# Kernel optimization log

Hardware: AMD Instinct MI355X
Metric: run time of the kernel (lower is better)

The kernel has to match this reference:

```python
import jax, jax.numpy as jnp
import numpy as np

N_STEPS, BATCH, N_IN, N_NEURONS, N_OUT = 512, 256, 64, 256, 1


def setup_inputs() -> dict:
    key = jax.random.key(0)
    ks = jax.random.split(key, 12)
    s_in = 1.0 / np.sqrt(N_NEURONS)
    inp = {
        "X": jax.random.normal(ks[0], (N_STEPS, BATCH, N_IN), jnp.float32),
        # nn.RNN (tanh, 1 layer) params
        "W_ih": jax.random.uniform(ks[1], (N_NEURONS, N_IN), jnp.float32, -s_in, s_in),
        "W_hh": jax.random.uniform(ks[2], (N_NEURONS, N_NEURONS), jnp.float32, -s_in, s_in),
        "b_ih": jax.random.uniform(ks[3], (N_NEURONS,), jnp.float32, -s_in, s_in),
        "b_hh": jax.random.uniform(ks[4], (N_NEURONS,), jnp.float32, -s_in, s_in),
        # nn.RNNCell params
        "Wc_ih": jax.random.uniform(ks[5], (N_NEURONS, N_NEURONS), jnp.float32, -s_in, s_in),
        "Wc_hh": jax.random.uniform(ks[6], (N_NEURONS, N_NEURONS), jnp.float32, -s_in, s_in),
        "bc_ih": jax.random.uniform(ks[7], (N_NEURONS,), jnp.float32, -s_in, s_in),
        "bc_hh": jax.random.uniform(ks[8], (N_NEURONS,), jnp.float32, -s_in, s_in),
        # fc params
        "W_fc": jax.random.uniform(ks[9], (N_OUT, N_NEURONS), jnp.float32, -s_in, s_in),
        "b_fc": jax.random.uniform(ks[10], (N_OUT,), jnp.float32, -s_in, s_in),
    }
    return inp


def reference(X, W_ih, W_hh, b_ih, b_hh, Wc_ih, Wc_hh, bc_ih, bc_hh, W_fc, b_fc):
    batch = X.shape[1]
    n_neurons = W_hh.shape[0]

    # --- rnn_pre: single-layer tanh RNN over time (h0 = zeros) ---
    def rnn_step(h, x_t):
        h_new = jnp.tanh(x_t @ W_ih.T + b_ih + h @ W_hh.T + b_hh)
        return h_new, h_new

    h0 = jnp.zeros((batch, n_neurons), X.dtype)
    _, out_pre = jax.lax.scan(rnn_step, h0, X)  # (S, B, N)

    # --- attention loop, n_neurons iterations, sequential dependency ---
    def att_step(hp, _):
        # pre_soft = sum(out_pre * hidden_post, 2) -> (S, B)
        pre_soft = jnp.einsum("sbn,bn->sb", out_pre, hp)
        # softmax over dim 0 (time)
        post_soft = jax.nn.softmax(pre_soft, axis=0)
        # attention = sum over time of out_pre weighted by post_soft -> (B, N)
        attention = jnp.einsum("sbn,sb->bn", out_pre, post_soft)
        # torch call rnn_cell_post(hidden_post, attention): input=hp, hx=attention
        hp_new = jnp.tanh(hp @ Wc_ih.T + bc_ih + attention @ Wc_hh.T + bc_hh)
        return hp_new, None

    hp0 = jnp.zeros((batch, n_neurons), X.dtype)
    hidden_post, _ = jax.lax.scan(att_step, hp0, None, length=n_neurons)

    return hidden_post @ W_fc.T + b_fc  # (B, n_outputs)
```

## Files before the change

### kernel.cpp

```cpp
#include <hip/hip_runtime.h>
#include <hip/hip_fp16.h>
#include <math.h>

#define NSTEPS 512
#define BATCH  256
#define NIN    64
#define NN     256

__device__ __forceinline__ void gll16(const void* gp, void* lp) {
    __builtin_amdgcn_global_load_lds(
        (const __attribute__((address_space(1))) void*)gp,
        (__attribute__((address_space(3))) void*)lp, 16, 0, 0);
}

extern "C" __global__ void pack_kernel(const float* __restrict__ Wc_ih,
                                       const float* __restrict__ Wc_hh,
                                       uint2* __restrict__ W4T)
{
    const int n = blockIdx.x, t = threadIdx.x;
    {
        float4 v = ((const float4*)(Wc_ih + n * NN))[t];
        __half2 a = __floats2half2_rn(v.x, v.y);
        __half2 c = __floats2half2_rn(v.z, v.w);
        uint2 o; o.x = *(uint32_t*)&a; o.y = *(uint32_t*)&c;
        W4T[t * 256 + n] = o;
    }
    {
        float4 v = ((const float4*)(Wc_hh + n * NN))[t];
        __half2 a = __floats2half2_rn(v.x, v.y);
        __half2 c = __floats2half2_rn(v.z, v.w);
        uint2 o; o.x = *(uint32_t*)&a; o.y = *(uint32_t*)&c;
        W4T[(64 + t) * 256 + n] = o;
    }
}

extern "C" __global__ void __launch_bounds__(1024, 4)
rnn_kernel(const float* __restrict__ X, const float* __restrict__ W_ih,
           const float* __restrict__ W_hh, const float* __restrict__ b_ih,
           const float* __restrict__ b_hh, __half* __restrict__ A2)
{
    const int b = blockIdx.x, t = threadIdx.x;
    const int n = t & 255, kq = t >> 8;

    __shared__ float h_lds[NN];
    __shared__ float x_lds[NIN];
    __shared__ float part[4 * NN];

    float wih[16];
#pragma unroll
    for (int j = 0; j < 16; ++j) wih[j] = W_ih[n * NIN + kq * 16 + j];
    float whh[64];
#pragma unroll
    for (int j = 0; j < 64; ++j) whh[j] = W_hh[n * NN + kq * 64 + j];
    const float bias = b_ih[n] + b_hh[n];

    float xr = (t < NIN) ? X[b * NIN + t] : 0.f;
    if (t < NN) h_lds[t] = 0.f;
    __syncthreads();

    __half2* Ab2 = (__half2*)(A2 + (size_t)b * NSTEPS * NN);

    for (int s = 0; s < NSTEPS; ++s) {
        if (t < NIN) x_lds[t] = xr;
        __syncthreads();
        if (t < NIN && s + 1 < NSTEPS) xr = X[((s + 1) * BATCH + b) * NIN + t];

        float a0 = 0.f, a1 = 0.f;
#pragma unroll
        for (int j = 0; j < 16; ++j) a0 = fmaf(wih[j], x_lds[kq * 16 + j], a0);
#pragma unroll
        for (int j = 0; j < 64; ++j) a1 = fmaf(whh[j], h_lds[kq * 64 + j], a1);
        part[kq * NN + n] = a0 + a1;
        __syncthreads();
        if (t < NN) {
            const float hn = tanhf(part[t] + part[NN + t] + part[2 * NN + t] +
                                   part[3 * NN + t] + bias);
            h_lds[t] = hn;
            const float hn1 = __shfl_down(hn, 1);
            if (!(t & 1)) Ab2[s * (NN / 2) + (t >> 1)] = __floats2half2_rn(hn, hn1);
        }
        __syncthreads();
    }
}

#define AW2     16384
#define HP_PAD  68
#define LDS_FLOATS (2*AW2 + 272 + 272 + 2048 + 128 + 128)
#define LDS_BYTES  (LDS_FLOATS * 4)

extern "C" __global__ void __launch_bounds__(512, 2)
attn_kernel(const __half* __restrict__ A2, const uint2* __restrict__ W4T,
            const float* __restrict__ bc_ih, const float* __restrict__ bc_hh,
            const float* __restrict__ W_fc, const float* __restrict__ b_fc,
            float* __restrict__ out)
{
    extern __shared__ float sm[];
    uint32_t* aw      = (uint32_t*)sm;
    float*    hp_lds  = sm + 2 * AW2;
    float*    att_lds = hp_lds + 272;
    float*    attp    = att_lds + 272;
    float*    pre_lds = attp + 2048;
    float*    e_lds   = pre_lds + 128;

    const int b    = blockIdx.x;
    const int t    = threadIdx.x;
    const int lane = t & 63;
    const int w    = t >> 6;

    const int pe = t & 7, pr = t >> 3;
    const int un = t & 255, um = t >> 8;
    const float bcs = (t < 256) ? (bc_ih[un] + bc_hh[un]) : 0.f;

    if (t < 256) hp_lds[(t >> 6) * HP_PAD + (t & 63)] = 0.f;

    const char* Abyte = (const char*)(A2 + (size_t)b * NSTEPS * NN);
    int soff[8];
#pragma unroll
    for (int i = 0; i < 8; ++i) {
        const int row = 16 * w + 2 * i + (lane >> 5);
        soff[i] = row * 512 + (((lane & 31) ^ (row & 7)) << 4);
    }

#pragma unroll
    for (int i = 0; i < 8; ++i)
        gll16(Abyte + soff[i], (char*)aw + (w * 8 + i) * 1024);
    __syncthreads();

    for (int it = 0; it < NN; ++it) {
        float hpr[32];
        {
            const float* hb = hp_lds + (pe >> 1) * HP_PAD + (pe & 1) * 32;
#pragma unroll
            for (int j = 0; j < 8; ++j) {
                float4 v = *(const float4*)&hb[4 * j];
                hpr[4*j] = v.x; hpr[4*j+1] = v.y; hpr[4*j+2] = v.z; hpr[4*j+3] = v.w;
            }
        }

        float m = -INFINITY, l = 0.f, acc_ih = 0.f;
        float att4[4] = {0.f, 0.f, 0.f, 0.f};

        for (int c = 0; c < 4; ++c) {
            const uint32_t* ab = aw + (c & 1) * AW2;

            {
                const char* src = Abyte + (((c + 1) & 3) << 16);
                char* dst = (char*)(aw + (~c & 1) * AW2);
#pragma unroll
                for (int i = 0; i < 8; ++i)
                    gll16(src + soff[i], dst + (w * 8 + i) * 1024);
            }

#pragma unroll
            for (int pass = 0; pass < 2; ++pass) {
                const int r = pass * 64 + pr;
                const uint32_t* arow = ab + r * 128;
                const int sw = (r & 7) << 2;
                float acc = 0.f;
#pragma unroll
                for (int jj = 0; jj < 4; ++jj) {
                    uint4 wv = *(const uint4*)&arow[(pe * 16 + 4 * jj) ^ sw];
                    float2 f0 = __half22float2(*(__half2*)&wv.x);
                    float2 f1 = __half22float2(*(__half2*)&wv.y);
                    float2 f2 = __half22float2(*(__half2*)&wv.z);
                    float2 f3 = __half22float2(*(__half2*)&wv.w);
                    acc = fmaf(f0.x, hpr[8*jj+0], acc);
                    acc = fmaf(f0.y, hpr[8*jj+1], acc);
                    acc = fmaf(f1.x, hpr[8*jj+2], acc);
                    acc = fmaf(f1.y, hpr[8*jj+3], acc);
                    acc = fmaf(f2.x, hpr[8*jj+4], acc);
                    acc = fmaf(f2.y, hpr[8*jj+5], acc);
                    acc = fmaf(f3.x, hpr[8*jj+6], acc);
                    acc = fmaf(f3.y, hpr[8*jj+7], acc);
                }
                acc += __shfl_xor(acc, 1);
                acc += __shfl_xor(acc, 2);
                acc += __shfl_xor(acc, 4);
                if (pe == 0) pre_lds[r] = acc;
            }
            __syncthreads();

            {
                const float p0 = pre_lds[lane], p1 = pre_lds[64 + lane];
                float v = fmaxf(p0, p1);
#pragma unroll
                for (int o = 32; o > 0; o >>= 1) v = fmaxf(v, __shfl_xor(v, o));
                const float newm = fmaxf(m, v);
                const float rs   = expf(m - newm);
                const float e0 = expf(p0 - newm), e1 = expf(p1 - newm);
                float sv = e0 + e1;
#pragma unroll
                for (int o = 32; o > 0; o >>= 1) sv += __shfl_xor(sv, o);
                l = l * rs + sv;
                m = newm;
                if (w == 0) { e_lds[lane] = e0; e_lds[64 + lane] = e1; }
#pragma unroll
                for (int j = 0; j < 4; ++j) att4[j] *= rs;
            }
            __syncthreads();

            {
#pragma unroll
                for (int i = 0; i < 16; ++i) {
                    const int r = w * 16 + i;
                    const float e = e_lds[r];
                    uint2 wv = *(const uint2*)&ab[r * 128 + ((2 * lane) ^ ((r & 7) << 2))];
                    float2 f0 = __half22float2(*(__half2*)&wv.x);
                    float2 f1 = __half22float2(*(__half2*)&wv.y);
                    att4[0] = fmaf(e, f0.x, att4[0]);
                    att4[1] = fmaf(e, f0.y, att4[1]);
                    att4[2] = fmaf(e, f1.x, att4[2]);
                    att4[3] = fmaf(e, f1.y, att4[3]);
                }
            }

            {
#pragma unroll
                for (int j = 0; j < 8; ++j) {
                    const int kq = um * 32 + c * 8 + j;
                    uint2 ww = W4T[kq * 256 + un];
                    float4 v = *(const float4*)&hp_lds[(kq >> 4) * HP_PAD + ((kq << 2) & 63)];
                    float2 f0 = __half22float2(*(__half2*)&ww.x);
                    float2 f1 = __half22float2(*(__half2*)&ww.y);
                    acc_ih = fmaf(f0.x, v.x, acc_ih);
                    acc_ih = fmaf(f0.y, v.y, acc_ih);
                    acc_ih = fmaf(f1.x, v.z, acc_ih);
                    acc_ih = fmaf(f1.y, v.w, acc_ih);
                }
            }
            __syncthreads();
        }

        *(float4*)&attp[w * 256 + 4 * lane] =
            make_float4(att4[0], att4[1], att4[2], att4[3]);
        __syncthreads();
        if (t < 256) {
            float s = 0.f;
#pragma unroll
            for (int sh = 0; sh < 8; ++sh) s += attp[sh * 256 + t];
            att_lds[(t >> 6) * HP_PAD + (t & 63)] = s;
        }
        __syncthreads();

        {
            float acc_hh = 0.f;
#pragma unroll
            for (int j = 0; j < 32; ++j) {
                const int kq = um * 32 + j;
                uint2 ww = W4T[(64 + kq) * 256 + un];
                float4 v = *(const float4*)&att_lds[(kq >> 4) * HP_PAD + ((kq << 2) & 63)];
                float2 f0 = __half22float2(*(__half2*)&ww.x);
                float2 f1 = __half22float2(*(__half2*)&ww.y);
                acc_hh = fmaf(f0.x, v.x, acc_hh);
                acc_hh = fmaf(f0.y, v.y, acc_hh);
                acc_hh = fmaf(f1.x, v.z, acc_hh);
                acc_hh = fmaf(f1.y, v.w, acc_hh);
            }
            attp[um * 256 + un] = acc_ih + acc_hh * (1.f / l);
        }
        __syncthreads();
        if (t < 256) {
            const float hn = tanhf(attp[t] + attp[256 + t] + bcs);
            hp_lds[(t >> 6) * HP_PAD + (t & 63)] = hn;
        }
        __syncthreads();
    }

    float v = (t < 256) ? hp_lds[(t >> 6) * HP_PAD + (t & 63)] * W_fc[un] : 0.f;
#pragma unroll
    for (int o = 32; o > 0; o >>= 1) v += __shfl_xor(v, o);
    if (lane == 0) attp[w] = v;
    __syncthreads();
    if (t == 0) {
        float s = b_fc[0];
#pragma unroll
        for (int q = 0; q < 8; ++q) s += attp[q];
        out[b] = s;
    }
}

extern "C" void kernel_launch(void* const* d_in, const int* in_sizes, int n_in,
                              void* d_out, int out_size, void* d_ws, size_t ws_size,
                              hipStream_t stream) {
    const float* X     = (const float*)d_in[0];
    const float* W_ih  = (const float*)d_in[1];
    const float* W_hh  = (const float*)d_in[2];
    const float* b_ih  = (const float*)d_in[3];
    const float* b_hh  = (const float*)d_in[4];
    const float* Wc_ih = (const float*)d_in[5];
    const float* Wc_hh = (const float*)d_in[6];
    const float* bc_ih = (const float*)d_in[7];
    const float* bc_hh = (const float*)d_in[8];
    const float* W_fc  = (const float*)d_in[9];
    const float* b_fc  = (const float*)d_in[10];
    float* out = (float*)d_out;

    __half* A2  = (__half*)d_ws;
    uint2*  W4T = (uint2*)((char*)d_ws + (size_t)64 * 1024 * 1024);

    hipFuncSetAttribute((const void*)attn_kernel,
                        hipFuncAttributeMaxDynamicSharedMemorySize, LDS_BYTES);

    pack_kernel<<<256, 64, 0, stream>>>(Wc_ih, Wc_hh, W4T);
    rnn_kernel<<<BATCH, 1024, 0, stream>>>(X, W_ih, W_hh, b_ih, b_hh, A2);
    attn_kernel<<<BATCH, 512, LDS_BYTES, stream>>>(A2, W4T, bc_ih, bc_hh,
                                                   W_fc, b_fc, out);
}
```

Baseline: 9.531 ms.

## Keep per-batch attention matrix resident in registers instead of streaming through LDS

```diff
diff --git a/kernel.cpp b/kernel.cpp
--- a/kernel.cpp
+++ b/kernel.cpp
@@ -7,10 +7,14 @@
 #define NIN    64
 #define NN     256
 
-__device__ __forceinline__ void gll16(const void* gp, void* lp) {
-    __builtin_amdgcn_global_load_lds(
-        (const __attribute__((address_space(1))) void*)gp,
-        (__attribute__((address_space(3))) void*)lp, 16, 0, 0);
+__device__ __forceinline__ float2 h2f(uint32_t u) {
+    __half2 h; *(uint32_t*)&h = u; return __half22float2(h);
+}
+
+template<int CTRL>
+__device__ __forceinline__ float dpp_add(float v) {
+    int p = __builtin_amdgcn_update_dpp(0, __float_as_int(v), CTRL, 0xF, 0xF, true);
+    return v + __int_as_float(p);
 }
 
 extern "C" __global__ void pack_kernel(const float* __restrict__ Wc_ih,
@@ -83,10 +87,30 @@
     }
 }
 
-#define AW2     16384
-#define HP_PAD  68
-#define LDS_FLOATS (2*AW2 + 272 + 272 + 2048 + 128 + 128)
-#define LDS_BYTES  (LDS_FLOATS * 4)
+__device__ __forceinline__ float dot16(uint4 wa, uint4 wb, const float* hpr) {
+    float a = 0.f; float2 f;
+    f = h2f(wa.x); a = fmaf(f.x, hpr[0],  a); a = fmaf(f.y, hpr[1],  a);
+    f = h2f(wa.y); a = fmaf(f.x, hpr[2],  a); a = fmaf(f.y, hpr[3],  a);
+    f = h2f(wa.z); a = fmaf(f.x, hpr[4],  a); a = fmaf(f.y, hpr[5],  a);
+    f = h2f(wa.w); a = fmaf(f.x, hpr[6],  a); a = fmaf(f.y, hpr[7],  a);
+    f = h2f(wb.x); a = fmaf(f.x, hpr[8],  a); a = fmaf(f.y, hpr[9],  a);
+    f = h2f(wb.y); a = fmaf(f.x, hpr[10], a); a = fmaf(f.y, hpr[11], a);
+    f = h2f(wb.z); a = fmaf(f.x, hpr[12], a); a = fmaf(f.y, hpr[13], a);
+    f = h2f(wb.w); a = fmaf(f.x, hpr[14], a); a = fmaf(f.y, hpr[15], a);
+    return a;
+}
+
+__device__ __forceinline__ void axpy16(float e, uint4 wa, uint4 wb, float* ap) {
+    float2 f;
+    f = h2f(wa.x); ap[0]  = fmaf(e, f.x, ap[0]);  ap[1]  = fmaf(e, f.y, ap[1]);
+    f = h2f(wa.y); ap[2]  = fmaf(e, f.x, ap[2]);  ap[3]  = fmaf(e, f.y, ap[3]);
+    f = h2f(wa.z); ap[4]  = fmaf(e, f.x, ap[4]);  ap[5]  = fmaf(e, f.y, ap[5]);
+    f = h2f(wa.w); ap[6]  = fmaf(e, f.x, ap[6]);  ap[7]  = fmaf(e, f.y, ap[7]);
+    f = h2f(wb.x); ap[8]  = fmaf(e, f.x, ap[8]);  ap[9]  = fmaf(e, f.y, ap[9]);
+    f = h2f(wb.y); ap[10] = fmaf(e, f.x, ap[10]); ap[11] = fmaf(e, f.y, ap[11]);
+    f = h2f(wb.z); ap[12] = fmaf(e, f.x, ap[12]); ap[13] = fmaf(e, f.y, ap[13]);
+    f = h2f(wb.w); ap[14] = fmaf(e, f.x, ap[14]); ap[15] = fmaf(e, f.y, ap[15]);
+}
 
 extern "C" __global__ void __launch_bounds__(512, 2)
 attn_kernel(const __half* __restrict__ A2, const uint2* __restrict__ W4T,
@@ -94,187 +118,156 @@
             const float* __restrict__ W_fc, const float* __restrict__ b_fc,
             float* __restrict__ out)
 {
-    extern __shared__ float sm[];
-    uint32_t* aw      = (uint32_t*)sm;
-    float*    hp_lds  = sm + 2 * AW2;
-    float*    att_lds = hp_lds + 272;
-    float*    attp    = att_lds + 272;
-    float*    pre_lds = attp + 2048;
-    float*    e_lds   = pre_lds + 128;
+    __shared__ float hp_pad[320];
+    __shared__ float at_pad[320];
+    __shared__ float att_part[8 * 320];
+    __shared__ float wred[8];
+    __shared__ float wsum[8];
+    __shared__ float mvih[256];
 
     const int b    = blockIdx.x;
     const int t    = threadIdx.x;
     const int lane = t & 63;
     const int w    = t >> 6;
-
-    const int pe = t & 7, pr = t >> 3;
-    const int un = t & 255, um = t >> 8;
-    const float bcs = (t < 256) ? (bc_ih[un] + bc_hh[un]) : 0.f;
-
-    if (t < 256) hp_lds[(t >> 6) * HP_PAD + (t & 63)] = 0.f;
-
-    const char* Abyte = (const char*)(A2 + (size_t)b * NSTEPS * NN);
-    int soff[8];
-#pragma unroll
-    for (int i = 0; i < 8; ++i) {
-        const int row = 16 * w + 2 * i + (lane >> 5);
-        soff[i] = row * 512 + (((lane & 31) ^ (row & 7)) << 4);
-    }
-
-#pragma unroll
-    for (int i = 0; i < 8; ++i)
-        gll16(Abyte + soff[i], (char*)aw + (w * 8 + i) * 1024);
+    const int sr   = lane >> 4;
+    const int nc   = lane & 15;
+    const int un   = t & 255;
+    const float bcs = bc_ih[un] + bc_hh[un];
+
+    uint4 areg[32];
+    {
+        const uint4* gA = (const uint4*)(A2 + (size_t)b * NSTEPS * NN);
+        const int rbase = w * 64 + sr * 16;
+#pragma unroll
+        for (int i = 0; i < 16; ++i) {
+            areg[2 * i]     = gA[(rbase + i) * 32 + nc * 2];
+            areg[2 * i + 1] = gA[(rbase + i) * 32 + nc * 2 + 1];
+        }
+    }
+
+    if (t < 256) hp_pad[(t >> 4) * 20 + (t & 15)] = 0.f;
     __syncthreads();
 
+    float a_hh = 0.f;
+
     for (int it = 0; it < NN; ++it) {
-        float hpr[32];
+        float hpr[16];
         {
-            const float* hb = hp_lds + (pe >> 1) * HP_PAD + (pe & 1) * 32;
-#pragma unroll
-            for (int j = 0; j < 8; ++j) {
-                float4 v = *(const float4*)&hb[4 * j];
-                hpr[4*j] = v.x; hpr[4*j+1] = v.y; hpr[4*j+2] = v.z; hpr[4*j+3] = v.w;
+            const float4* hq = (const float4*)&hp_pad[nc * 20];
+#pragma unroll
+            for (int k = 0; k < 4; ++k) {
+                float4 v = hq[k];
+                hpr[4*k] = v.x; hpr[4*k+1] = v.y; hpr[4*k+2] = v.z; hpr[4*k+3] = v.w;
             }
         }
 
-        float m = -INFINITY, l = 0.f, acc_ih = 0.f;
-        float att4[4] = {0.f, 0.f, 0.f, 0.f};
-
-        for (int c = 0; c < 4; ++c) {
-            const uint32_t* ab = aw + (c & 1) * AW2;
-
-            {
-                const char* src = Abyte + (((c + 1) & 3) << 16);
-                char* dst = (char*)(aw + (~c & 1) * AW2);
-#pragma unroll
-                for (int i = 0; i < 8; ++i)
-                    gll16(src + soff[i], dst + (w * 8 + i) * 1024);
+        float prep[16];
+#pragma unroll
+        for (int i = 0; i < 16; ++i)
+            prep[i] = dot16(areg[2 * i], areg[2 * i + 1], hpr);
+
+#pragma unroll
+        for (int i = 0; i < 16; ++i) {
+            prep[i] = dpp_add<0xB1>(prep[i]);
+            prep[i] = dpp_add<0x4E>(prep[i]);
+            prep[i] = dpp_add<0x141>(prep[i]);
+            prep[i] = dpp_add<0x128>(prep[i]);
+        }
+
+        float mx = prep[0];
+#pragma unroll
+        for (int i = 1; i < 16; ++i) mx = fmaxf(mx, prep[i]);
+        mx = fmaxf(mx, __shfl_xor(mx, 16));
+        mx = fmaxf(mx, __shfl_xor(mx, 32));
+        if (lane == 0) wred[w] = mx;
+        __syncthreads();
+        float gm = wred[0];
+#pragma unroll
+        for (int q = 1; q < 8; ++q) gm = fmaxf(gm, wred[q]);
+
+        float er[16], ls = 0.f;
+#pragma unroll
+        for (int i = 0; i < 16; ++i) { er[i] = __expf(prep[i] - gm); ls += er[i]; }
+        ls += __shfl_xor(ls, 16);
+        ls += __shfl_xor(ls, 32);
+        if (lane == 0) wsum[w] = ls;
+
+        float attp[16];
+#pragma unroll
+        for (int j = 0; j < 16; ++j) attp[j] = 0.f;
+#pragma unroll
+        for (int i = 0; i < 16; ++i)
+            axpy16(er[i], areg[2 * i], areg[2 * i + 1], attp);
+#pragma unroll
+        for (int j = 0; j < 16; ++j) {
+            attp[j] += __shfl_xor(attp[j], 16);
+            attp[j] += __shfl_xor(attp[j], 32);
+        }
+        if (sr == 0) {
+            float4* dst = (float4*)&att_part[w * 320 + nc * 20];
+#pragma unroll
+            for (int k = 0; k < 4; ++k)
+                dst[k] = make_float4(attp[4*k], attp[4*k+1], attp[4*k+2], attp[4*k+3]);
+        }
+        __syncthreads();
+
+        float l = wsum[0];
+#pragma unroll
+        for (int q = 1; q < 8; ++q) l += wsum[q];
+
+        if (t < 256) {
+            const int g = t >> 4, r = t & 15;
+            float s = 0.f;
+#pragma unroll
+            for (int q = 0; q < 8; ++q) s += att_part[q * 320 + g * 20 + r];
+            at_pad[g * 20 + r] = s;
+        }
+        __syncthreads();
+
+        {
+            const uint2* Wp = W4T + (t >= 256 ? 0 : 64 * 256) + un;
+            const float* xp = (t >= 256) ? hp_pad : at_pad;
+            float a0 = 0.f, a1 = 0.f, a2 = 0.f, a3 = 0.f;
+#pragma unroll
+            for (int g = 0; g < 16; ++g) {
+                uint2 w0 = Wp[(4 * g + 0) * 256];
+                uint2 w1 = Wp[(4 * g + 1) * 256];
+                uint2 w2 = Wp[(4 * g + 2) * 256];
+                uint2 w3 = Wp[(4 * g + 3) * 256];
+                const float4* xg = (const float4*)&xp[g * 20];
+                float4 x0 = xg[0], x1 = xg[1], x2 = xg[2], x3 = xg[3];
+                float2 f;
+                f = h2f(w0.x); a0 = fmaf(f.x, x0.x, a0); a0 = fmaf(f.y, x0.y, a0);
+                f = h2f(w0.y); a0 = fmaf(f.x, x0.z, a0); a0 = fmaf(f.y, x0.w, a0);
+                f = h2f(w1.x); a1 = fmaf(f.x, x1.x, a1); a1 = fmaf(f.y, x1.y, a1);
+                f = h2f(w1.y); a1 = fmaf(f.x, x1.z, a1); a1 = fmaf(f.y, x1.w, a1);
+                f = h2f(w2.x); a2 = fmaf(f.x, x2.x, a2); a2 = fmaf(f.y, x2.y, a2);
+                f = h2f(w2.y); a2 = fmaf(f.x, x2.z, a2); a2 = fmaf(f.y, x2.w, a2);
+                f = h2f(w3.x); a3 = fmaf(f.x, x3.x, a3); a3 = fmaf(f.y, x3.y, a3);
+                f = h2f(w3.y); a3 = fmaf(f.x, x3.z, a3); a3 = fmaf(f.y, x3.w, a3);
             }
-
-#pragma unroll
-            for (int pass = 0; pass < 2; ++pass) {
-                const int r = pass * 64 + pr;
-                const uint32_t* arow = ab + r * 128;
-                const int sw = (r & 7) << 2;
-                float acc = 0.f;
-#pragma unroll
-                for (int jj = 0; jj < 4; ++jj) {
-                    uint4 wv = *(const uint4*)&arow[(pe * 16 + 4 * jj) ^ sw];
-                    float2 f0 = __half22float2(*(__half2*)&wv.x);
-                    float2 f1 = __half22float2(*(__half2*)&wv.y);
-                    float2 f2 = __half22float2(*(__half2*)&wv.z);
-                    float2 f3 = __half22float2(*(__half2*)&wv.w);
-                    acc = fmaf(f0.x, hpr[8*jj+0], acc);
-                    acc = fmaf(f0.y, hpr[8*jj+1], acc);
-                    acc = fmaf(f1.x, hpr[8*jj+2], acc);
-                    acc = fmaf(f1.y, hpr[8*jj+3], acc);
-                    acc = fmaf(f2.x, hpr[8*jj+4], acc);
-                    acc = fmaf(f2.y, hpr[8*jj+5], acc);
-                    acc = fmaf(f3.x, hpr[8*jj+6], acc);
-                    acc = fmaf(f3.y, hpr[8*jj+7], acc);
-                }
-                acc += __shfl_xor(acc, 1);
-                acc += __shfl_xor(acc, 2);
-                acc += __shfl_xor(acc, 4);
-                if (pe == 0) pre_lds[r] = acc;
-            }
-            __syncthreads();
-
-            {
-                const float p0 = pre_lds[lane], p1 = pre_lds[64 + lane];
-                float v = fmaxf(p0, p1);
-#pragma unroll
-                for (int o = 32; o > 0; o >>= 1) v = fmaxf(v, __shfl_xor(v, o));
-                const float newm = fmaxf(m, v);
-                const float rs   = expf(m - newm);
-                const float e0 = expf(p0 - newm), e1 = expf(p1 - newm);
-                float sv = e0 + e1;
-#pragma unroll
-                for (int o = 32; o > 0; o >>= 1) sv += __shfl_xor(sv, o);
-                l = l * rs + sv;
-                m = newm;
-                if (w == 0) { e_lds[lane] = e0; e_lds[64 + lane] = e1; }
-#pragma unroll
-                for (int j = 0; j < 4; ++j) att4[j] *= rs;
-            }
-            __syncthreads();
-
-            {
-#pragma unroll
-                for (int i = 0; i < 16; ++i) {
-                    const int r = w * 16 + i;
-                    const float e = e_lds[r];
-                    uint2 wv = *(const uint2*)&ab[r * 128 + ((2 * lane) ^ ((r & 7) << 2))];
-                    float2 f0 = __half22float2(*(__half2*)&wv.x);
-                    float2 f1 = __half22float2(*(__half2*)&wv.y);
-                    att4[0] = fmaf(e, f0.x, att4[0]);
-                    att4[1] = fmaf(e, f0.y, att4[1]);
-                    att4[2] = fmaf(e, f1.x, att4[2]);
-                    att4[3] = fmaf(e, f1.y, att4[3]);
-                }
-            }
-
-            {
-#pragma unroll
-                for (int j = 0; j < 8; ++j) {
-                    const int kq = um * 32 + c * 8 + j;
-                    uint2 ww = W4T[kq * 256 + un];
-                    float4 v = *(const float4*)&hp_lds[(kq >> 4) * HP_PAD + ((kq << 2) & 63)];
-                    float2 f0 = __half22float2(*(__half2*)&ww.x);
-                    float2 f1 = __half22float2(*(__half2*)&ww.y);
-                    acc_ih = fmaf(f0.x, v.x, acc_ih);
-                    acc_ih = fmaf(f0.y, v.y, acc_ih);
-                    acc_ih = fmaf(f1.x, v.z, acc_ih);
-                    acc_ih = fmaf(f1.y, v.w, acc_ih);
-                }
-            }
-            __syncthreads();
-        }
-
-        *(float4*)&attp[w * 256 + 4 * lane] =
-            make_float4(att4[0], att4[1], att4[2], att4[3]);
-        __syncthreads();
+            const float acc = (a0 + a1) + (a2 + a3);
+            if (t >= 256) mvih[un] = acc;
+            else          a_hh = acc;
+        }
+        __syncthreads();
+
         if (t < 256) {
-            float s = 0.f;
-#pragma unroll
-            for (int sh = 0; sh < 8; ++sh) s += attp[sh * 256 + t];
-            att_lds[(t >> 6) * HP_PAD + (t & 63)] = s;
-        }
-        __syncthreads();
-
-        {
-            float acc_hh = 0.f;
-#pragma unroll
-            for (int j = 0; j < 32; ++j) {
-                const int kq = um * 32 + j;
-                uint2 ww = W4T[(64 + kq) * 256 + un];
-                float4 v = *(const float4*)&att_lds[(kq >> 4) * HP_PAD + ((kq << 2) & 63)];
-                float2 f0 = __half22float2(*(__half2*)&ww.x);
-                float2 f1 = __half22float2(*(__half2*)&ww.y);
-                acc_hh = fmaf(f0.x, v.x, acc_hh);
-                acc_hh = fmaf(f0.y, v.y, acc_hh);
-                acc_hh = fmaf(f1.x, v.z, acc_hh);
-                acc_hh = fmaf(f1.y, v.w, acc_hh);
-            }
-            attp[um * 256 + un] = acc_ih + acc_hh * (1.f / l);
-        }
-        __syncthreads();
-        if (t < 256) {
-            const float hn = tanhf(attp[t] + attp[256 + t] + bcs);
-            hp_lds[(t >> 6) * HP_PAD + (t & 63)] = hn;
-        }
-        __syncthreads();
-    }
-
-    float v = (t < 256) ? hp_lds[(t >> 6) * HP_PAD + (t & 63)] * W_fc[un] : 0.f;
+            const float hn = tanhf(mvih[t] + a_hh / l + bcs);
+            hp_pad[(t >> 4) * 20 + (t & 15)] = hn;
+        }
+        __syncthreads();
+    }
+
+    float v = (t < 256) ? hp_pad[(t >> 4) * 20 + (t & 15)] * W_fc[un] : 0.f;
 #pragma unroll
     for (int o = 32; o > 0; o >>= 1) v += __shfl_xor(v, o);
-    if (lane == 0) attp[w] = v;
+    if (lane == 0) wred[w] = v;
     __syncthreads();
     if (t == 0) {
         float s = b_fc[0];
 #pragma unroll
-        for (int q = 0; q < 8; ++q) s += attp[q];
+        for (int q = 0; q < 8; ++q) s += wred[q];
         out[b] = s;
     }
 }
@@ -298,11 +291,8 @@
     __half* A2  = (__half*)d_ws;
     uint2*  W4T = (uint2*)((char*)d_ws + (size_t)64 * 1024 * 1024);
 
-    hipFuncSetAttribute((const void*)attn_kernel,
-                        hipFuncAttributeMaxDynamicSharedMemorySize, LDS_BYTES);
-
     pack_kernel<<<256, 64, 0, stream>>>(Wc_ih, Wc_hh, W4T);
     rnn_kernel<<<BATCH, 1024, 0, stream>>>(X, W_ih, W_hh, b_ih, b_hh, A2);
-    attn_kernel<<<BATCH, 512, LDS_BYTES, stream>>>(A2, W4T, bc_ih, bc_hh,
-                                                   W_fc, b_fc, out);
-}
+    attn_kernel<<<BATCH, 512, 0, stream>>>(A2, W4T, bc_ih, bc_hh,
+                                           W_fc, b_fc, out);
+}
```

Result: slower. 15.54 ms (+63.0%).
